# Kernel optimization log

Hardware: AMD Instinct MI355X
Metric: run time of the kernel (lower is better)

Reference implementation:

```python
import jax, jax.numpy as jnp
import numpy as np

DIM = 1024
NUM_EXPERTS = 8
N_TOKENS = 8192


def setup_inputs() -> dict:
    key = jax.random.key(0)
    ks = jax.random.split(key, 6)
    z_real = jax.random.normal(ks[0], (N_TOKENS, DIM), dtype=jnp.float32)
    z_imag = jax.random.normal(ks[1], (N_TOKENS, DIM), dtype=jnp.float32)
    # gate: nn.Linear(2*dim, E) -> weight [E, 2*dim], bias [E]
    Wg = jax.random.normal(ks[2], (NUM_EXPERTS, 2 * DIM), dtype=jnp.float32) * (1.0 / np.sqrt(2 * DIM))
    bg = jnp.zeros((NUM_EXPERTS,), dtype=jnp.float32)
    # experts: per-expert real/imag square weights [E, dim, dim] (nn.Linear layout: [out, in])
    Wr = jax.random.normal(ks[3], (NUM_EXPERTS, DIM, DIM), dtype=jnp.float32) * (1.0 / np.sqrt(DIM))
    Wi = jax.random.normal(ks[4], (NUM_EXPERTS, DIM, DIM), dtype=jnp.float32) * (1.0 / np.sqrt(DIM))
    return {"z_real": z_real, "z_imag": z_imag, "Wg": Wg, "bg": bg, "Wr": Wr, "Wi": Wi}


def reference(z_real, z_imag, Wg, bg, Wr, Wi):
    # gate over concat(real, imag)
    z_flat = jnp.concatenate([z_real, z_imag], axis=-1)            # [N, 2D]
    gates = jax.nn.softmax(z_flat @ Wg.T + bg, axis=-1)            # [N, E]
    # all-expert complex linear: y = x @ W^T with W [E, out, in]
    rr = jnp.einsum('ni,eoi->neo', z_real, Wr)                     # real @ Wr
    ii = jnp.einsum('ni,eoi->neo', z_imag, Wi)                     # imag @ Wi
    ri = jnp.einsum('ni,eoi->neo', z_imag, Wr)                     # imag @ Wr
    ir = jnp.einsum('ni,eoi->neo', z_real, Wi)                     # real @ Wi
    out_r = jnp.einsum('ne,neo->no', gates, rr - ii)               # [N, D]
    out_i = jnp.einsum('ne,neo->no', gates, ri + ir)               # [N, D]
    return jnp.stack([out_r, out_i], axis=0)                       # [2, N, D]
```

## Files before the change

### kernel.cpp

```cpp
#include <hip/hip_runtime.h>
#include <hip/hip_bf16.h>

#define NTOK 8192
#define DIM 1024
#define NEXP 8
#define NT 256
#define BK 64

typedef float f32x4 __attribute__((ext_vector_type(4)));
typedef short s16x8 __attribute__((ext_vector_type(8)));
typedef unsigned short u16;
typedef unsigned short u16x4 __attribute__((ext_vector_type(4)));

__device__ __forceinline__ u16 f2bf(float f) {
    __hip_bfloat16 h = __float2bfloat16(f);
    return *reinterpret_cast<u16*>(&h);
}
__device__ __forceinline__ float bf2f(u16 u) {
    unsigned v = ((unsigned)u) << 16;
    return __uint_as_float(v);
}

#define GLOAD16(gsrc, ldst)                                                     \
    __builtin_amdgcn_global_load_lds(                                           \
        (const __attribute__((address_space(1))) void*)(gsrc),                  \
        (__attribute__((address_space(3))) void*)(ldst), 16, 0, 0)

#define MFMA16(a, b, c) __builtin_amdgcn_mfma_f32_16x16x32_bf16((a), (b), (c), 0, 0, 0)

__global__ __launch_bounds__(256) void gates_kernel(
    const float* __restrict__ zr, const float* __restrict__ zi,
    const float* __restrict__ Wg, const float* __restrict__ bg,
    float* __restrict__ gates)
{
    const int wave = threadIdx.x >> 6, lane = threadIdx.x & 63;
    const int n = blockIdx.x * 4 + wave;

    float v[32];
    const float* zrp = zr + (size_t)n * DIM;
    const float* zip = zi + (size_t)n * DIM;
#pragma unroll
    for (int j = 0; j < 16; ++j) v[j] = zrp[j * 64 + lane];
#pragma unroll
    for (int j = 0; j < 16; ++j) v[16 + j] = zip[j * 64 + lane];

    float s[NEXP];
#pragma unroll
    for (int e = 0; e < NEXP; ++e) {
        const float* wrow = Wg + (size_t)e * (2 * DIM);
        float a = 0.f;
#pragma unroll
        for (int j = 0; j < 32; ++j) a += v[j] * wrow[j * 64 + lane];
#pragma unroll
        for (int m = 32; m; m >>= 1) a += __shfl_xor(a, m);
        s[e] = a + bg[e];
    }
    float mx = s[0];
#pragma unroll
    for (int e = 1; e < NEXP; ++e) mx = fmaxf(mx, s[e]);
    float p[NEXP], sum = 0.f;
#pragma unroll
    for (int e = 0; e < NEXP; ++e) { p[e] = expf(s[e] - mx); sum += p[e]; }
    const float inv = 1.f / sum;
    if (lane == 0) {
#pragma unroll
        for (int e = 0; e < NEXP; ++e) gates[(size_t)n * NEXP + e] = p[e] * inv;
    }
}

__global__ __launch_bounds__(256) void cvt4_kernel(
    const float* __restrict__ zr, const float* __restrict__ zi,
    const float* __restrict__ Wr, const float* __restrict__ Wi,
    u16* __restrict__ zr16, u16* __restrict__ zi16,
    u16* __restrict__ Wr16, u16* __restrict__ Wi16)
{
    const size_t total = (size_t)NEXP * DIM * DIM / 4;
    for (size_t i = (size_t)blockIdx.x * 256 + threadIdx.x; i < total;
         i += (size_t)gridDim.x * 256) {
        f32x4 a = ((const f32x4*)zr)[i];
        f32x4 b = ((const f32x4*)zi)[i];
        f32x4 c = ((const f32x4*)Wr)[i];
        f32x4 d = ((const f32x4*)Wi)[i];
        u16x4 pa, pb, pc, pd;
#pragma unroll
        for (int j = 0; j < 4; ++j) {
            pa[j] = f2bf(a[j]); pb[j] = f2bf(b[j]);
            pc[j] = f2bf(c[j]); pd[j] = f2bf(d[j]);
        }
        ((u16x4*)zr16)[i] = pa;
        ((u16x4*)zi16)[i] = pb;
        ((u16x4*)Wr16)[i] = pc;
        ((u16x4*)Wi16)[i] = pd;
    }
}

__global__ __launch_bounds__(512, 2) void moe_gemm5(
    const u16* __restrict__ zr16, const u16* __restrict__ zi16,
    const u16* __restrict__ Wr16, const u16* __restrict__ Wi16,
    const float* __restrict__ gates, float* __restrict__ out)
{
    extern __shared__ u16 lds[];

    const int linear = blockIdx.x + 32 * (blockIdx.y + 4 * blockIdx.z);
    const int grp = linear & 7;
    const int bm = linear >> 3;
    const int bn = grp & 3;
    const int sel = grp >> 2;

    const int tid = threadIdx.x;
    const int lane = tid & 63;
    const int wid = tid >> 6;
    const int wr = wid >> 2;
    const int wc = wid & 3;

    const int srow = tid >> 3;
    const int schunk = (tid & 7) ^ (srow & 7);
    int arow[4], gidx[4], brow[4];
#pragma unroll
    for (int j = 0; j < 4; ++j) {
        const int gr = bm * 256 + srow + j * 64;
        arow[j] = gr * DIM + schunk * 8;
        gidx[j] = gr * NEXP;
        brow[j] = (bn * 256 + srow + j * 64) * DIM + schunk * 8;
    }

    const int cg = lane >> 4;
    const int l7 = lane & 7;
    const int ach0 = (cg ^ l7) * 8;
    const int ach1 = ((4 + cg) ^ l7) * 8;
    const int arbase = (wr * 128 + (lane & 15)) * BK;
    const int brbase = 16384 + (wc * 64 + (lane & 15)) * BK;

    f32x4 acc[8][4];
#pragma unroll
    for (int m = 0; m < 8; ++m)
#pragma unroll
        for (int n = 0; n < 4; ++n) acc[m][n] = (f32x4){0.f, 0.f, 0.f, 0.f};

    const u16* Asrc = sel ? zi16 : zr16;
    const u16* Bseg = Wr16;
    float sg[4];
#pragma unroll
    for (int j = 0; j < 4; ++j) sg[j] = gates[gidx[j]];

    {
        s16x8 ga[4];
#pragma unroll
        for (int j = 0; j < 4; ++j) ga[j] = *(const s16x8*)(Asrc + arow[j]);
#pragma unroll
        for (int i = 0; i < 4; ++i)
            GLOAD16(Bseg + brow[i], &lds[16384 + (i * 512 + tid) * 8]);
#pragma unroll
        for (int j = 0; j < 4; ++j) {
            s16x8 w;
#pragma unroll
            for (int q = 0; q < 8; ++q)
                w[q] = (short)f2bf(bf2f((u16)ga[j][q]) * sg[j]);
            *(s16x8*)&lds[(tid + j * 512) * 8] = w;
        }
        asm volatile("s_waitcnt vmcnt(0) lgkmcnt(0)" ::: "memory");
        __syncthreads();
    }

    int buf = 0;
#pragma unroll 1
    for (int t = 0; t < NT; ++t) {
        const int tn = t + 1;
        if ((tn & 15) == 0) {
            const int seg = tn >> 4;
            const int e = (seg >> 1) & 7;
            const int half = seg & 1;
            Asrc = (half ^ sel) ? zi16 : zr16;
            Bseg = (half ? Wi16 : Wr16) + (size_t)e * DIM * DIM;
            const float sgn = (sel == 0 && half == 1) ? -1.f : 1.f;
#pragma unroll
            for (int j = 0; j < 4; ++j) sg[j] = sgn * gates[gidx[j] + e];
        }
        const int kb = (tn & 15) << 6;
        const int ab = (buf << 15) + arbase;
        const int bb = (buf << 15) + brbase;
        const int sb = (buf ^ 1) << 15;

        s16x8 ga[4];
#pragma unroll
        for (int j = 0; j < 4; ++j) ga[j] = *(const s16x8*)(Asrc + arow[j] + kb);
        GLOAD16(Bseg + brow[0] + kb, &lds[sb + 16384 + (0 * 512 + tid) * 8]);
        GLOAD16(Bseg + brow[1] + kb, &lds[sb + 16384 + (1 * 512 + tid) * 8]);
        GLOAD16(Bseg + brow[2] + kb, &lds[sb + 16384 + (2 * 512 + tid) * 8]);
        GLOAD16(Bseg + brow[3] + kb, &lds[sb + 16384 + (3 * 512 + tid) * 8]);
        s16x8 bf0[4], bf1[4], afr[4];
#pragma unroll
        for (int n = 0; n < 4; ++n) bf0[n] = *(const s16x8*)&lds[bb + n * 1024 + ach0];
#pragma unroll
        for (int m = 0; m < 4; ++m) afr[m] = *(const s16x8*)&lds[ab + m * 1024 + ach0];
        __builtin_amdgcn_s_barrier();
        __builtin_amdgcn_s_setprio(1);
#pragma unroll
        for (int m = 0; m < 4; ++m)
#pragma unroll
            for (int n = 0; n < 4; ++n) acc[m][n] = MFMA16(afr[m], bf0[n], acc[m][n]);
        __builtin_amdgcn_s_setprio(0);
        __builtin_amdgcn_s_barrier();

#pragma unroll
        for (int m = 0; m < 4; ++m) afr[m] = *(const s16x8*)&lds[ab + (m + 4) * 1024 + ach0];
        __builtin_amdgcn_s_barrier();
        __builtin_amdgcn_s_setprio(1);
#pragma unroll
        for (int m = 0; m < 4; ++m)
#pragma unroll
            for (int n = 0; n < 4; ++n) acc[m + 4][n] = MFMA16(afr[m], bf0[n], acc[m + 4][n]);
#pragma unroll
        for (int j = 0; j < 2; ++j) {
            s16x8 w;
#pragma unroll
            for (int q = 0; q < 8; ++q)
                w[q] = (short)f2bf(bf2f((u16)ga[j][q]) * sg[j]);
            *(s16x8*)&lds[sb + (tid + j * 512) * 8] = w;
        }
        __builtin_amdgcn_s_setprio(0);
        __builtin_amdgcn_s_barrier();

#pragma unroll
        for (int n = 0; n < 4; ++n) bf1[n] = *(const s16x8*)&lds[bb + n * 1024 + ach1];
#pragma unroll
        for (int m = 0; m < 4; ++m) afr[m] = *(const s16x8*)&lds[ab + m * 1024 + ach1];
        __builtin_amdgcn_s_barrier();
        __builtin_amdgcn_s_setprio(1);
#pragma unroll
        for (int m = 0; m < 4; ++m)
#pragma unroll
            for (int n = 0; n < 4; ++n) acc[m][n] = MFMA16(afr[m], bf1[n], acc[m][n]);
#pragma unroll
        for (int j = 2; j < 4; ++j) {
            s16x8 w;
#pragma unroll
            for (int q = 0; q < 8; ++q)
                w[q] = (short)f2bf(bf2f((u16)ga[j][q]) * sg[j]);
            *(s16x8*)&lds[sb + (tid + j * 512) * 8] = w;
        }
        __builtin_amdgcn_s_setprio(0);
        __builtin_amdgcn_s_barrier();

#pragma unroll
        for (int m = 0; m < 4; ++m) afr[m] = *(const s16x8*)&lds[ab + (m + 4) * 1024 + ach1];
        __builtin_amdgcn_s_barrier();
        __builtin_amdgcn_s_setprio(1);
#pragma unroll
        for (int m = 0; m < 4; ++m)
#pragma unroll
            for (int n = 0; n < 4; ++n) acc[m + 4][n] = MFMA16(afr[m], bf1[n], acc[m + 4][n]);
        __builtin_amdgcn_s_setprio(0);
        asm volatile("s_waitcnt vmcnt(0) lgkmcnt(0)" ::: "memory");
        __builtin_amdgcn_s_barrier();

        buf ^= 1;
    }

    float* op = out + (size_t)sel * NTOK * DIM;
    const int col0 = bn * 256 + wc * 64 + (lane & 15);
    const int row0 = bm * 256 + wr * 128 + ((lane >> 4) << 2);
#pragma unroll
    for (int m = 0; m < 8; ++m)
#pragma unroll
        for (int n = 0; n < 4; ++n)
#pragma unroll
            for (int j = 0; j < 4; ++j)
                op[(size_t)(row0 + m * 16 + j) * DIM + col0 + n * 16] = acc[m][n][j];
}

extern "C" void kernel_launch(void* const* d_in, const int* in_sizes, int n_in,
                              void* d_out, int out_size, void* d_ws, size_t ws_size,
                              hipStream_t stream) {
    const float* zr = (const float*)d_in[0];
    const float* zi = (const float*)d_in[1];
    const float* Wg = (const float*)d_in[2];
    const float* bg = (const float*)d_in[3];
    const float* Wr = (const float*)d_in[4];
    const float* Wi = (const float*)d_in[5];
    float* out = (float*)d_out;

    const size_t NELEM = (size_t)NEXP * DIM * DIM;
    u16* zr16 = (u16*)d_ws;
    u16* zi16 = zr16 + NELEM;
    u16* Wr16 = zi16 + NELEM;
    u16* Wi16 = Wr16 + NELEM;
    float* gates = (float*)(Wi16 + NELEM);

    cvt4_kernel<<<2048, 256, 0, stream>>>(zr, zi, Wr, Wi, zr16, zi16, Wr16, Wi16);
    gates_kernel<<<NTOK / 4, 256, 0, stream>>>(zr, zi, Wg, bg, gates);

    hipFuncSetAttribute((const void*)moe_gemm5,
                        hipFuncAttributeMaxDynamicSharedMemorySize, 131072);
    dim3 grid(NTOK / 256, DIM / 256, 2);
    moe_gemm5<<<grid, 512, 131072, stream>>>(zr16, zi16, Wr16, Wi16, gates, out);
}
```

Measured before the change: 612.1 us.

## Triple-buffer B tiles in LDS with two-step-ahead prefetch

Expands B-operand LDS staging from double to triple buffering and issues the global-to-LDS B loads two k-steps ahead, waiting only for the older batch via vmcnt(4). The A tile keeps double buffering with its own index. This aims to hide global memory latency for weight loads better, at the cost of raising dynamic LDS to 160KB per block and adding modular buffer indexing.

```diff
diff --git a/kernel.cpp b/kernel.cpp
--- a/kernel.cpp
+++ b/kernel.cpp
@@ -94,7 +94,7 @@
     }
 }
 
-__global__ __launch_bounds__(512, 2) void moe_gemm5(
+__global__ __launch_bounds__(512, 2) void moe_gemm6(
     const u16* __restrict__ zr16, const u16* __restrict__ zi16,
     const u16* __restrict__ Wr16, const u16* __restrict__ Wi16,
     const float* __restrict__ gates, float* __restrict__ out)
@@ -129,7 +129,7 @@
     const int ach0 = (cg ^ l7) * 8;
     const int ach1 = ((4 + cg) ^ l7) * 8;
     const int arbase = (wr * 128 + (lane & 15)) * BK;
-    const int brbase = 16384 + (wc * 64 + (lane & 15)) * BK;
+    const int brbase = (wc * 64 + (lane & 15)) * BK;
 
     f32x4 acc[8][4];
 #pragma unroll
@@ -149,7 +149,10 @@
         for (int j = 0; j < 4; ++j) ga[j] = *(const s16x8*)(Asrc + arow[j]);
 #pragma unroll
         for (int i = 0; i < 4; ++i)
-            GLOAD16(Bseg + brow[i], &lds[16384 + (i * 512 + tid) * 8]);
+            GLOAD16(Bseg + brow[i], &lds[32768 + (i * 512 + tid) * 8]);
+#pragma unroll
+        for (int i = 0; i < 4; ++i)
+            GLOAD16(Bseg + brow[i] + 64, &lds[32768 + 16384 + (i * 512 + tid) * 8]);
 #pragma unroll
         for (int j = 0; j < 4; ++j) {
             s16x8 w;
@@ -158,36 +161,45 @@
                 w[q] = (short)f2bf(bf2f((u16)ga[j][q]) * sg[j]);
             *(s16x8*)&lds[(tid + j * 512) * 8] = w;
         }
-        asm volatile("s_waitcnt vmcnt(0) lgkmcnt(0)" ::: "memory");
+        asm volatile("s_waitcnt vmcnt(4) lgkmcnt(0)" ::: "memory");
         __syncthreads();
     }
 
-    int buf = 0;
+    int br = 0;
 #pragma unroll 1
     for (int t = 0; t < NT; ++t) {
-        const int tn = t + 1;
-        if ((tn & 15) == 0) {
-            const int seg = tn >> 4;
+        const int tn1 = t + 1, tn2 = t + 2;
+        if ((tn1 & 15) == 0) {
+            const int seg = tn1 >> 4;
             const int e = (seg >> 1) & 7;
             const int half = seg & 1;
             Asrc = (half ^ sel) ? zi16 : zr16;
-            Bseg = (half ? Wi16 : Wr16) + (size_t)e * DIM * DIM;
             const float sgn = (sel == 0 && half == 1) ? -1.f : 1.f;
 #pragma unroll
             for (int j = 0; j < 4; ++j) sg[j] = sgn * gates[gidx[j] + e];
         }
-        const int kb = (tn & 15) << 6;
-        const int ab = (buf << 15) + arbase;
-        const int bb = (buf << 15) + brbase;
-        const int sb = (buf ^ 1) << 15;
+        if ((tn2 & 15) == 0) {
+            const int seg = tn2 >> 4;
+            const int e = (seg >> 1) & 7;
+            const int half = seg & 1;
+            Bseg = ((seg & 1) ? Wi16 : Wr16) + (size_t)e * DIM * DIM;
+            (void)half;
+        }
+        const int ka = (tn1 & 15) << 6;
+        const int kb = (tn2 & 15) << 6;
+        const int bs = (br + 2) % 3;
+        const int ab = ((t & 1) << 14) + arbase;
+        const int bb = 32768 + br * 16384 + brbase;
+        const int sa = ((tn1 & 1) << 14);
+        const int sbB = 32768 + bs * 16384;
 
         s16x8 ga[4];
 #pragma unroll
-        for (int j = 0; j < 4; ++j) ga[j] = *(const s16x8*)(Asrc + arow[j] + kb);
-        GLOAD16(Bseg + brow[0] + kb, &lds[sb + 16384 + (0 * 512 + tid) * 8]);
-        GLOAD16(Bseg + brow[1] + kb, &lds[sb + 16384 + (1 * 512 + tid) * 8]);
-        GLOAD16(Bseg + brow[2] + kb, &lds[sb + 16384 + (2 * 512 + tid) * 8]);
-        GLOAD16(Bseg + brow[3] + kb, &lds[sb + 16384 + (3 * 512 + tid) * 8]);
+        for (int j = 0; j < 4; ++j) ga[j] = *(const s16x8*)(Asrc + arow[j] + ka);
+        GLOAD16(Bseg + brow[0] + kb, &lds[sbB + (0 * 512 + tid) * 8]);
+        GLOAD16(Bseg + brow[1] + kb, &lds[sbB + (1 * 512 + tid) * 8]);
+        GLOAD16(Bseg + brow[2] + kb, &lds[sbB + (2 * 512 + tid) * 8]);
+        GLOAD16(Bseg + brow[3] + kb, &lds[sbB + (3 * 512 + tid) * 8]);
         s16x8 bf0[4], bf1[4], afr[4];
 #pragma unroll
         for (int n = 0; n < 4; ++n) bf0[n] = *(const s16x8*)&lds[bb + n * 1024 + ach0];
@@ -216,7 +228,7 @@
 #pragma unroll
             for (int q = 0; q < 8; ++q)
                 w[q] = (short)f2bf(bf2f((u16)ga[j][q]) * sg[j]);
-            *(s16x8*)&lds[sb + (tid + j * 512) * 8] = w;
+            *(s16x8*)&lds[sa + (tid + j * 512) * 8] = w;
         }
         __builtin_amdgcn_s_setprio(0);
         __builtin_amdgcn_s_barrier();
@@ -237,7 +249,7 @@
 #pragma unroll
             for (int q = 0; q < 8; ++q)
                 w[q] = (short)f2bf(bf2f((u16)ga[j][q]) * sg[j]);
-            *(s16x8*)&lds[sb + (tid + j * 512) * 8] = w;
+            *(s16x8*)&lds[sa + (tid + j * 512) * 8] = w;
         }
         __builtin_amdgcn_s_setprio(0);
         __builtin_amdgcn_s_barrier();
@@ -251,11 +263,12 @@
 #pragma unroll
             for (int n = 0; n < 4; ++n) acc[m + 4][n] = MFMA16(afr[m], bf1[n], acc[m + 4][n]);
         __builtin_amdgcn_s_setprio(0);
-        asm volatile("s_waitcnt vmcnt(0) lgkmcnt(0)" ::: "memory");
-        __builtin_amdgcn_s_barrier();
-
-        buf ^= 1;
-    }
+        asm volatile("s_waitcnt vmcnt(4) lgkmcnt(0)" ::: "memory");
+        __builtin_amdgcn_s_barrier();
+
+        br = (br == 2) ? 0 : br + 1;
+    }
+    asm volatile("s_waitcnt vmcnt(0)" ::: "memory");
 
     float* op = out + (size_t)sel * NTOK * DIM;
     const int col0 = bn * 256 + wc * 64 + (lane & 15);
@@ -290,8 +303,8 @@
     cvt4_kernel<<<2048, 256, 0, stream>>>(zr, zi, Wr, Wi, zr16, zi16, Wr16, Wi16);
     gates_kernel<<<NTOK / 4, 256, 0, stream>>>(zr, zi, Wg, bg, gates);
 
-    hipFuncSetAttribute((const void*)moe_gemm5,
-                        hipFuncAttributeMaxDynamicSharedMemorySize, 131072);
+    hipFuncSetAttribute((const void*)moe_gemm6,
+                        hipFuncAttributeMaxDynamicSharedMemorySize, 163840);
     dim3 grid(NTOK / 256, DIM / 256, 2);
-    moe_gemm5<<<grid, 512, 131072, stream>>>(zr16, zi16, Wr16, Wi16, gates, out);
-}
+    moe_gemm6<<<grid, 512, 163840, stream>>>(zr16, zi16, Wr16, Wi16, gates, out);
+}
```

Result: no change. 614.9 us (+0.5%).

## Use 4-wave blocks with 128x128 per-wave tiles and XCD-aware block mapping

Applied to the files above, without the earlier changes.

The GEMM kernel moves from 512-thread blocks (8 waves, 128x64 wave tiles) to 256-thread blocks (4 waves, 128x128 wave tiles), one block per CU. The per-wave MFMA-to-LDS-read ratio doubles, and most intra-iteration s_barriers are replaced with sched_barriers. Blocks are remapped on a 1D grid so that each XCD handles a contiguous set of M tiles, which is meant to improve L2 reuse. The costs are a 256-float accumulator per thread, which may spill or limit occupancy, and less latency hiding with only four waves per CU.

```diff
diff --git a/kernel.cpp b/kernel.cpp
--- a/kernel.cpp
+++ b/kernel.cpp
@@ -6,6 +6,7 @@
 #define NEXP 8
 #define NT 256
 #define BK 64
+#define NELEMZ ((size_t)NTOK * DIM)
 
 typedef float f32x4 __attribute__((ext_vector_type(4)));
 typedef short s16x8 __attribute__((ext_vector_type(8)));
@@ -27,6 +28,7 @@
         (__attribute__((address_space(3))) void*)(ldst), 16, 0, 0)
 
 #define MFMA16(a, b, c) __builtin_amdgcn_mfma_f32_16x16x32_bf16((a), (b), (c), 0, 0, 0)
+#define SGB() __builtin_amdgcn_sched_barrier(0)
 
 __global__ __launch_bounds__(256) void gates_kernel(
     const float* __restrict__ zr, const float* __restrict__ zi,
@@ -74,7 +76,7 @@
     u16* __restrict__ zr16, u16* __restrict__ zi16,
     u16* __restrict__ Wr16, u16* __restrict__ Wi16)
 {
-    const size_t total = (size_t)NEXP * DIM * DIM / 4;
+    const size_t total = NELEMZ / 4;
     for (size_t i = (size_t)blockIdx.x * 256 + threadIdx.x; i < total;
          i += (size_t)gridDim.x * 256) {
         f32x4 a = ((const f32x4*)zr)[i];
@@ -94,176 +96,169 @@
     }
 }
 
-__global__ __launch_bounds__(512, 2) void moe_gemm5(
+__global__ __launch_bounds__(256, 1) void moe_gemm18(
     const u16* __restrict__ zr16, const u16* __restrict__ zi16,
     const u16* __restrict__ Wr16, const u16* __restrict__ Wi16,
     const float* __restrict__ gates, float* __restrict__ out)
 {
     extern __shared__ u16 lds[];
 
-    const int linear = blockIdx.x + 32 * (blockIdx.y + 4 * blockIdx.z);
-    const int grp = linear & 7;
-    const int bm = linear >> 3;
+    const int bid = blockIdx.x;
+    const int xcd = bid & 7;
+    const int bm = xcd * 4 + ((bid >> 3) & 3);
+    const int grp = bid >> 5;
     const int bn = grp & 3;
     const int sel = grp >> 2;
 
     const int tid = threadIdx.x;
     const int lane = tid & 63;
     const int wid = tid >> 6;
-    const int wr = wid >> 2;
-    const int wc = wid & 3;
-
-    const int srow = tid >> 3;
-    const int schunk = (tid & 7) ^ (srow & 7);
-    int arow[4], gidx[4], brow[4];
-#pragma unroll
-    for (int j = 0; j < 4; ++j) {
-        const int gr = bm * 256 + srow + j * 64;
-        arow[j] = gr * DIM + schunk * 8;
-        gidx[j] = gr * NEXP;
-        brow[j] = (bn * 256 + srow + j * 64) * DIM + schunk * 8;
+    const int wr = wid >> 1;
+    const int wc = wid & 1;
+
+    int a_goff[8], gidx[8], b_goff[8];
+#pragma unroll
+    for (int q = 0; q < 8; ++q) {
+        const int idx = q * 256 + tid;
+        const int row = idx >> 3;
+        const int c = (idx & 7) ^ (row & 7);
+        a_goff[q] = (bm * 256 + row) * DIM + c * 8;
+        gidx[q] = (bm * 256 + row) * NEXP;
+        b_goff[q] = (bn * 256 + row) * DIM + c * 8;
     }
 
     const int cg = lane >> 4;
     const int l7 = lane & 7;
     const int ach0 = (cg ^ l7) * 8;
     const int ach1 = ((4 + cg) ^ l7) * 8;
-    const int arbase = (wr * 128 + (lane & 15)) * BK;
-    const int brbase = 16384 + (wc * 64 + (lane & 15)) * BK;
-
-    f32x4 acc[8][4];
+    const int abase = (wr * 128 + (lane & 15)) * BK;
+    const int bbase = (wc * 128 + (lane & 15)) * BK;
+
+    f32x4 acc[8][8];
 #pragma unroll
     for (int m = 0; m < 8; ++m)
 #pragma unroll
-        for (int n = 0; n < 4; ++n) acc[m][n] = (f32x4){0.f, 0.f, 0.f, 0.f};
+        for (int n = 0; n < 8; ++n) acc[m][n] = (f32x4){0.f, 0.f, 0.f, 0.f};
 
     const u16* Asrc = sel ? zi16 : zr16;
     const u16* Bseg = Wr16;
-    float sg[4];
-#pragma unroll
-    for (int j = 0; j < 4; ++j) sg[j] = gates[gidx[j]];
+    float sg[8];
+#pragma unroll
+    for (int q = 0; q < 8; ++q) sg[q] = gates[gidx[q]];
 
     {
-        s16x8 ga[4];
-#pragma unroll
-        for (int j = 0; j < 4; ++j) ga[j] = *(const s16x8*)(Asrc + arow[j]);
-#pragma unroll
-        for (int i = 0; i < 4; ++i)
-            GLOAD16(Bseg + brow[i], &lds[16384 + (i * 512 + tid) * 8]);
-#pragma unroll
-        for (int j = 0; j < 4; ++j) {
+        s16x8 ga[8];
+#pragma unroll
+        for (int q = 0; q < 8; ++q) ga[q] = *(const s16x8*)(Asrc + a_goff[q]);
+#pragma unroll
+        for (int q = 0; q < 8; ++q)
+            GLOAD16(Bseg + b_goff[q], &lds[32768 + (q * 256 + tid) * 8]);
+#pragma unroll
+        for (int q = 0; q < 8; ++q) {
             s16x8 w;
 #pragma unroll
-            for (int q = 0; q < 8; ++q)
-                w[q] = (short)f2bf(bf2f((u16)ga[j][q]) * sg[j]);
-            *(s16x8*)&lds[(tid + j * 512) * 8] = w;
+            for (int e = 0; e < 8; ++e)
+                w[e] = (short)f2bf(bf2f((u16)ga[q][e]) * sg[q]);
+            *(s16x8*)&lds[(q * 256 + tid) * 8] = w;
         }
         asm volatile("s_waitcnt vmcnt(0) lgkmcnt(0)" ::: "memory");
-        __syncthreads();
-    }
-
-    int buf = 0;
+        __builtin_amdgcn_s_barrier();
+    }
+
 #pragma unroll 1
     for (int t = 0; t < NT; ++t) {
-        const int tn = t + 1;
-        if ((tn & 15) == 0) {
-            const int seg = tn >> 4;
+        const int t1 = t + 1;
+        if ((t1 & 15) == 0) {
+            const int seg = t1 >> 4;
             const int e = (seg >> 1) & 7;
             const int half = seg & 1;
             Asrc = (half ^ sel) ? zi16 : zr16;
             Bseg = (half ? Wi16 : Wr16) + (size_t)e * DIM * DIM;
             const float sgn = (sel == 0 && half == 1) ? -1.f : 1.f;
 #pragma unroll
-            for (int j = 0; j < 4; ++j) sg[j] = sgn * gates[gidx[j] + e];
-        }
-        const int kb = (tn & 15) << 6;
-        const int ab = (buf << 15) + arbase;
-        const int bb = (buf << 15) + brbase;
-        const int sb = (buf ^ 1) << 15;
-
-        s16x8 ga[4];
-#pragma unroll
-        for (int j = 0; j < 4; ++j) ga[j] = *(const s16x8*)(Asrc + arow[j] + kb);
-        GLOAD16(Bseg + brow[0] + kb, &lds[sb + 16384 + (0 * 512 + tid) * 8]);
-        GLOAD16(Bseg + brow[1] + kb, &lds[sb + 16384 + (1 * 512 + tid) * 8]);
-        GLOAD16(Bseg + brow[2] + kb, &lds[sb + 16384 + (2 * 512 + tid) * 8]);
-        GLOAD16(Bseg + brow[3] + kb, &lds[sb + 16384 + (3 * 512 + tid) * 8]);
-        s16x8 bf0[4], bf1[4], afr[4];
-#pragma unroll
-        for (int n = 0; n < 4; ++n) bf0[n] = *(const s16x8*)&lds[bb + n * 1024 + ach0];
-#pragma unroll
-        for (int m = 0; m < 4; ++m) afr[m] = *(const s16x8*)&lds[ab + m * 1024 + ach0];
-        __builtin_amdgcn_s_barrier();
+            for (int q = 0; q < 8; ++q) sg[q] = sgn * gates[gidx[q] + e];
+        }
+        const int ka = (t1 & 15) << 6;
+        const int rs = t & 1;
+        const int ab = rs * 16384 + abase;
+        const int bb = 32768 + rs * 16384 + bbase;
+        const int sa = (rs ^ 1) * 16384;
+        const int sb = 32768 + (rs ^ 1) * 16384;
+
+        s16x8 ga[8];
+#pragma unroll
+        for (int q = 0; q < 8; ++q) ga[q] = *(const s16x8*)(Asrc + a_goff[q] + ka);
+#pragma unroll
+        for (int q = 0; q < 8; ++q)
+            GLOAD16(Bseg + b_goff[q] + ka, &lds[sb + (q * 256 + tid) * 8]);
+
+        s16x8 a0[8], b0[8], a1[8], b1[8];
+#pragma unroll
+        for (int n = 0; n < 8; ++n) b0[n] = *(const s16x8*)&lds[bb + n * 1024 + ach0];
+#pragma unroll
+        for (int m = 0; m < 8; ++m) a0[m] = *(const s16x8*)&lds[ab + m * 1024 + ach0];
+        SGB();
         __builtin_amdgcn_s_setprio(1);
 #pragma unroll
         for (int m = 0; m < 4; ++m)
 #pragma unroll
-            for (int n = 0; n < 4; ++n) acc[m][n] = MFMA16(afr[m], bf0[n], acc[m][n]);
-        __builtin_amdgcn_s_setprio(0);
-        __builtin_amdgcn_s_barrier();
-
-#pragma unroll
-        for (int m = 0; m < 4; ++m) afr[m] = *(const s16x8*)&lds[ab + (m + 4) * 1024 + ach0];
-        __builtin_amdgcn_s_barrier();
+            for (int n = 0; n < 8; ++n) acc[m][n] = MFMA16(a0[m], b0[n], acc[m][n]);
+        __builtin_amdgcn_s_setprio(0);
+
+#pragma unroll
+        for (int n = 0; n < 8; ++n) b1[n] = *(const s16x8*)&lds[bb + n * 1024 + ach1];
+#pragma unroll
+        for (int m = 0; m < 8; ++m) a1[m] = *(const s16x8*)&lds[ab + m * 1024 + ach1];
+#pragma unroll
+        for (int q = 0; q < 4; ++q) {
+            s16x8 w;
+#pragma unroll
+            for (int e = 0; e < 8; ++e)
+                w[e] = (short)f2bf(bf2f((u16)ga[q][e]) * sg[q]);
+            *(s16x8*)&lds[sa + (q * 256 + tid) * 8] = w;
+        }
+        SGB();
+        __builtin_amdgcn_s_setprio(1);
+#pragma unroll
+        for (int m = 4; m < 8; ++m)
+#pragma unroll
+            for (int n = 0; n < 8; ++n) acc[m][n] = MFMA16(a0[m], b0[n], acc[m][n]);
+        __builtin_amdgcn_s_setprio(0);
+
+#pragma unroll
+        for (int q = 4; q < 8; ++q) {
+            s16x8 w;
+#pragma unroll
+            for (int e = 0; e < 8; ++e)
+                w[e] = (short)f2bf(bf2f((u16)ga[q][e]) * sg[q]);
+            *(s16x8*)&lds[sa + (q * 256 + tid) * 8] = w;
+        }
+        SGB();
         __builtin_amdgcn_s_setprio(1);
 #pragma unroll
         for (int m = 0; m < 4; ++m)
 #pragma unroll
-            for (int n = 0; n < 4; ++n) acc[m + 4][n] = MFMA16(afr[m], bf0[n], acc[m + 4][n]);
-#pragma unroll
-        for (int j = 0; j < 2; ++j) {
-            s16x8 w;
-#pragma unroll
-            for (int q = 0; q < 8; ++q)
-                w[q] = (short)f2bf(bf2f((u16)ga[j][q]) * sg[j]);
-            *(s16x8*)&lds[sb + (tid + j * 512) * 8] = w;
-        }
-        __builtin_amdgcn_s_setprio(0);
-        __builtin_amdgcn_s_barrier();
-
-#pragma unroll
-        for (int n = 0; n < 4; ++n) bf1[n] = *(const s16x8*)&lds[bb + n * 1024 + ach1];
-#pragma unroll
-        for (int m = 0; m < 4; ++m) afr[m] = *(const s16x8*)&lds[ab + m * 1024 + ach1];
-        __builtin_amdgcn_s_barrier();
-        __builtin_amdgcn_s_setprio(1);
-#pragma unroll
-        for (int m = 0; m < 4; ++m)
-#pragma unroll
-            for (int n = 0; n < 4; ++n) acc[m][n] = MFMA16(afr[m], bf1[n], acc[m][n]);
-#pragma unroll
-        for (int j = 2; j < 4; ++j) {
-            s16x8 w;
-#pragma unroll
-            for (int q = 0; q < 8; ++q)
-                w[q] = (short)f2bf(bf2f((u16)ga[j][q]) * sg[j]);
-            *(s16x8*)&lds[sb + (tid + j * 512) * 8] = w;
-        }
-        __builtin_amdgcn_s_setprio(0);
-        __builtin_amdgcn_s_barrier();
-
-#pragma unroll
-        for (int m = 0; m < 4; ++m) afr[m] = *(const s16x8*)&lds[ab + (m + 4) * 1024 + ach1];
-        __builtin_amdgcn_s_barrier();
-        __builtin_amdgcn_s_setprio(1);
-#pragma unroll
-        for (int m = 0; m < 4; ++m)
-#pragma unroll
-            for (int n = 0; n < 4; ++n) acc[m + 4][n] = MFMA16(afr[m], bf1[n], acc[m + 4][n]);
-        __builtin_amdgcn_s_setprio(0);
+            for (int n = 0; n < 8; ++n) acc[m][n] = MFMA16(a1[m], b1[n], acc[m][n]);
+        __builtin_amdgcn_s_setprio(0);
+        SGB();
+        __builtin_amdgcn_s_setprio(1);
+#pragma unroll
+        for (int m = 4; m < 8; ++m)
+#pragma unroll
+            for (int n = 0; n < 8; ++n) acc[m][n] = MFMA16(a1[m], b1[n], acc[m][n]);
+        __builtin_amdgcn_s_setprio(0);
+
         asm volatile("s_waitcnt vmcnt(0) lgkmcnt(0)" ::: "memory");
         __builtin_amdgcn_s_barrier();
-
-        buf ^= 1;
     }
 
     float* op = out + (size_t)sel * NTOK * DIM;
-    const int col0 = bn * 256 + wc * 64 + (lane & 15);
+    const int col0 = bn * 256 + wc * 128 + (lane & 15);
     const int row0 = bm * 256 + wr * 128 + ((lane >> 4) << 2);
 #pragma unroll
     for (int m = 0; m < 8; ++m)
 #pragma unroll
-        for (int n = 0; n < 4; ++n)
+        for (int n = 0; n < 8; ++n)
 #pragma unroll
             for (int j = 0; j < 4; ++j)
                 op[(size_t)(row0 + m * 16 + j) * DIM + col0 + n * 16] = acc[m][n][j];
@@ -280,18 +275,16 @@
     const float* Wi = (const float*)d_in[5];
     float* out = (float*)d_out;
 
-    const size_t NELEM = (size_t)NEXP * DIM * DIM;
     u16* zr16 = (u16*)d_ws;
-    u16* zi16 = zr16 + NELEM;
-    u16* Wr16 = zi16 + NELEM;
-    u16* Wi16 = Wr16 + NELEM;
-    float* gates = (float*)(Wi16 + NELEM);
+    u16* zi16 = zr16 + NELEMZ;
+    u16* Wr16 = zi16 + NELEMZ;
+    u16* Wi16 = Wr16 + NELEMZ;
+    float* gates = (float*)(Wi16 + NELEMZ);
 
     cvt4_kernel<<<2048, 256, 0, stream>>>(zr, zi, Wr, Wi, zr16, zi16, Wr16, Wi16);
     gates_kernel<<<NTOK / 4, 256, 0, stream>>>(zr, zi, Wg, bg, gates);
 
-    hipFuncSetAttribute((const void*)moe_gemm5,
+    hipFuncSetAttribute((const void*)moe_gemm18,
                         hipFuncAttributeMaxDynamicSharedMemorySize, 131072);
-    dim3 grid(NTOK / 256, DIM / 256, 2);
-    moe_gemm5<<<grid, 512, 131072, stream>>>(zr16, zi16, Wr16, Wi16, gates, out);
-}
+    moe_gemm18<<<256, 256, 131072, stream>>>(zr16, zi16, Wr16, Wi16, gates, out);
+}
```

Result: slower. 1.318 ms (+115.3%).
